# Performance work log

Measured on AMD Instinct MI355X. Metric: run time of the kernel, lower is better.

## Reference

```python
import jax, jax.numpy as jnp
import numpy as np

# ---- config constants (must match init_kwargs) ----
B, S, D, H, HD = 2, 2048, 512, 8, 64
N_BLK, L_BLK = 64, 32          # block_size, block_len (S = N_BLK*L_BLK)
R, RM = 8, 4                   # router_size, group_router_mul_factor
LN, GN, GE, GT = 8, 4, 16, 2   # moe layers, groups, group experts, topk per token
DR, DG = 128, 128
FFH = 1024
THETA = 10000.0
EPS = 1e-6

_INV_FREQ = (1.0 / THETA) ** (np.arange(0, HD, 2, dtype=np.float32) / HD)


def rmsnorm(x, w):
    return x * jax.lax.rsqrt(jnp.mean(x * x, axis=-1, keepdims=True) + EPS) * w


def rope(x):
    # x: (b, h, s, hd); y1 = x1*cos + x2*sin, y2 = -x1*sin + x2*cos (as in RotaryEmb)
    s = x.shape[2]
    freqs = jnp.outer(jnp.arange(s, dtype=jnp.float32), jnp.asarray(_INV_FREQ))[None, None]
    cos, sin = jnp.cos(freqs), jnp.sin(freqs)
    x1, x2 = jnp.split(x, 2, axis=-1)
    return jnp.concatenate([x1 * cos + x2 * sin, -x1 * sin + x2 * cos], axis=-1)


def layer(x, mask, qkv_w, o_w, up_w, down_w, n1, n2):
    b, s, d = x.shape
    xn = rmsnorm(x, n1)
    q, k, v = jnp.split(xn @ qkv_w, 3, axis=-1)
    sh = lambda t: t.reshape(b, s, H, HD).transpose(0, 2, 1, 3)  # b h s hd
    q, k, v = rope(sh(q)), rope(sh(k)), sh(v)
    scores = jnp.einsum('bhqa,bhka->bhqk', q, k) / np.sqrt(HD).astype(np.float32)
    if mask is not None:
        scores = jnp.where(mask[:, None], scores, -jnp.inf)
    p = jax.nn.softmax(scores, axis=-1)
    o = jnp.einsum('bhqk,bhka->bhqa', p, v).transpose(0, 2, 1, 3).reshape(b, s, d)
    x = x + o @ o_w
    xn2 = rmsnorm(x, n2)
    h1, h2 = jnp.split(xn2 @ up_w, 2, axis=-1)
    return x + (jax.nn.silu(h1) * h2) @ down_w


def _l2n(t, axis):
    return t / jnp.maximum(jnp.linalg.norm(t, axis=axis, keepdims=True), 1e-12)


def forward(x, doc, router_token, out_w, keys_router, keys_gate,
            enc_qkv, enc_o, enc_up, enc_down, enc_n1, enc_n2,
            rtr_qkv, rtr_o, rtr_up, rtr_down, rtr_n1, rtr_n2):
    # ---- AuxEncoder: block-causal AND same-document mask (global_attn branch) ----
    qb = jnp.arange(S) // N_BLK
    causal = qb[:, None] >= qb[None, :]                       # (S, S)
    mask = causal[None] & (doc[:, :, None] == doc[:, None, :])  # (B, S, S)
    for i in range(enc_qkv.shape[0]):
        x = layer(x, mask, enc_qkv[i], enc_o[i], enc_up[i], enc_down[i], enc_n1[i], enc_n2[i])

    # ---- AuxRouter: split into blocks, append router tokens, full attention ----
    xr = x.reshape(B * L_BLK, N_BLK, D)
    rt = jnp.broadcast_to(router_token, (B * L_BLK, R, D))
    xr = jnp.concatenate([xr, rt], axis=1)                    # (B*L, N+R, D)
    for i in range(rtr_qkv.shape[0]):
        xr = layer(xr, None, rtr_qkv[i], rtr_o[i], rtr_up[i], rtr_down[i], rtr_n1[i], rtr_n2[i])
    out = xr[:, N_BLK:] @ out_w                               # (B*L, R, DR+DG)
    xro, xgo = out[..., :DR], out[..., DR:]

    def expand(t, dd):
        # repeat '(b l) r d -> (r rm) b l d', roll(1, dim=2), flatten(1,2)
        t = t.reshape(B, L_BLK, R, dd).transpose(2, 0, 1, 3)  # (R, B, L, d)
        t = jnp.repeat(t, RM, axis=0)                          # (R*RM, B, L, d)
        t = jnp.roll(t, 1, axis=2)
        return t.reshape(R * RM, B * L_BLK, dd)

    xrr = _l2n(expand(xro, DR), -1)
    xgg = _l2n(expand(xgo, DG), -1)
    kr = _l2n(keys_router, 1)
    kg = _l2n(keys_gate, 1)
    rl = jnp.einsum('gbd,gde->gbe', xrr, kr)                  # (LN*GN, B*L, GE)
    gl = jnp.einsum('gbd,gde->gbe', xgg, kg)
    _, idx = jax.lax.top_k(rl, GT)                            # (LN*GN, B*L, GT)
    rv = jnp.take_along_axis(rl, idx, axis=-1)
    gv = jnp.take_along_axis(gl, idx, axis=-1)
    return jnp.stack([rv, gv], axis=0)                        # (2, 32, 64, 2)


def setup_inputs() -> dict:
    key = jax.random.key(0)
    ks = jax.random.split(key, 20)
    w = lambda k, shp: 0.02 * jax.random.normal(k, shp, dtype=jnp.float32)
    return {
        'x': jax.random.normal(ks[0], (B, S, D), dtype=jnp.float32),
        'doc': jnp.sort(jax.random.randint(ks[1], (B, S), 0, 4), axis=-1),
        'router_token': jax.random.normal(ks[2], (1, R, D), dtype=jnp.float32),
        'out_w': w(ks[3], (D, DR + DG)),
        'keys_router': jax.random.normal(ks[4], (LN * GN, DR, GE), dtype=jnp.float32),
        'keys_gate': jax.random.normal(ks[5], (LN * GN, DG, GE), dtype=jnp.float32),
        'enc_qkv': w(ks[6], (4, D, 3 * D)),
        'enc_o': w(ks[7], (4, D, D)),
        'enc_up': w(ks[8], (4, D, 2 * FFH)),
        'enc_down': w(ks[9], (4, FFH, D)),
        'enc_n1': jnp.ones((4, D), dtype=jnp.float32),
        'enc_n2': jnp.ones((4, D), dtype=jnp.float32),
        'rtr_qkv': w(ks[10], (2, D, 3 * D)),
        'rtr_o': w(ks[11], (2, D, D)),
        'rtr_up': w(ks[12], (2, D, 2 * FFH)),
        'rtr_down': w(ks[13], (2, FFH, D)),
        'rtr_n1': jnp.ones((2, D), dtype=jnp.float32),
        'rtr_n2': jnp.ones((2, D), dtype=jnp.float32),
    }


def reference(x, doc, router_token, out_w, keys_router, keys_gate,
              enc_qkv, enc_o, enc_up, enc_down, enc_n1, enc_n2,
              rtr_qkv, rtr_o, rtr_up, rtr_down, rtr_n1, rtr_n2):
    return forward(x, doc, router_token, out_w, keys_router, keys_gate,
                   enc_qkv, enc_o, enc_up, enc_down, enc_n1, enc_n2,
                   rtr_qkv, rtr_o, rtr_up, rtr_down, rtr_n1, rtr_n2)
```

## Files before the change

### kernel.cpp

```cpp
#include <hip/hip_runtime.h>
#include <hip/hip_bf16.h>
#include <cstdint>


typedef __attribute__((ext_vector_type(8))) short short8;
typedef __attribute__((ext_vector_type(4))) float f32x4;
typedef unsigned short ushort_t;

__device__ __forceinline__ float bf2f(unsigned short u) {
    return __uint_as_float(((unsigned)u) << 16);
}
__device__ __forceinline__ unsigned short f2bf(float f) {
    unsigned u = __float_as_uint(f);
    unsigned r = 0x7FFFu + ((u >> 16) & 1u);
    return (unsigned short)((u + r) >> 16);
}
__device__ __forceinline__ float wave_sum64(float v) {
#pragma unroll
    for (int o = 32; o; o >>= 1) v += __shfl_xor(v, o);
    return v;
}
__device__ __forceinline__ void load_lds16(const ushort_t* g, ushort_t* l) {
    __builtin_amdgcn_global_load_lds(
        (const __attribute__((address_space(1))) unsigned int*)g,
        (__attribute__((address_space(3))) unsigned int*)l, 16, 0, 0);
}

#define MFMA16(a, b, c) __builtin_amdgcn_mfma_f32_16x16x32_bf16(a, b, c, 0, 0, 0)
#define BARRIER_RAW() do { asm volatile("" ::: "memory"); \
    __builtin_amdgcn_s_barrier(); asm volatile("" ::: "memory"); } while (0)
#define VMCNT0() asm volatile("s_waitcnt vmcnt(0)" ::: "memory")

__global__ void copy_in_kernel(const float* __restrict__ src,
                               float* __restrict__ dst, int n) {
    int i = blockIdx.x * 256 + threadIdx.x;
    if (i < n) dst[i] = src[i];
}

__global__ __launch_bounds__(256) void wsplit_kernel(const float* __restrict__ W,
        unsigned short* __restrict__ WH, unsigned short* __restrict__ WL,
        int K, int N) {
    __shared__ float tile[32][33];
    int bn = blockIdx.x * 32, bk = blockIdx.y * 32;
    int tx = threadIdx.x & 31, ty = threadIdx.x >> 5;
#pragma unroll
    for (int i = 0; i < 4; ++i)
        tile[ty + 8 * i][tx] = W[(size_t)(bk + ty + 8 * i) * N + bn + tx];
    __syncthreads();
#pragma unroll
    for (int i = 0; i < 4; ++i) {
        int n = bn + ty + 8 * i, k = bk + tx;
        float x = tile[tx][ty + 8 * i];
        unsigned short h = f2bf(x);
        unsigned short lo = f2bf(x - bf2f(h));
        WH[(size_t)n * K + k] = h;
        WL[(size_t)n * K + k] = lo;
    }
}

__global__ __launch_bounds__(256) void rmsnorm_kernel(const float* __restrict__ X,
        const float* __restrict__ W, ushort_t* __restrict__ XNH,
        ushort_t* __restrict__ XNL) {
    int t = blockIdx.x, tid = threadIdx.x;
    const float* xr = X + (size_t)t * 512;
    float v0 = xr[tid], v1 = xr[tid + 256];
    float ss = wave_sum64(v0 * v0 + v1 * v1);
    __shared__ float red[4];
    if ((tid & 63) == 0) red[tid >> 6] = ss;
    __syncthreads();
    float tot = red[0] + red[1] + red[2] + red[3];
    float scale = rsqrtf(tot * (1.0f / 512.0f) + 1e-6f);
    float a0 = v0 * scale * W[tid];
    float a1 = v1 * scale * W[tid + 256];
    unsigned short h0 = f2bf(a0), h1 = f2bf(a1);
    size_t base = (size_t)t * 512;
    XNH[base + tid]       = h0;
    XNL[base + tid]       = f2bf(a0 - bf2f(h0));
    XNH[base + tid + 256] = h1;
    XNL[base + tid + 256] = f2bf(a1 - bf2f(h1));
}

template <int BM>
__global__ __launch_bounds__(256) void gemm3(
        const ushort_t* __restrict__ AH, const ushort_t* __restrict__ AL,
        const ushort_t* __restrict__ BH, const ushort_t* __restrict__ BL,
        const float* __restrict__ Res, float* __restrict__ C,
        int M, int N, int K) {
    constexpr int MI   = BM / 32;
    constexpr int ROWS = 2 * BM + 256;
    constexpr int LPW  = ROWS / 64;
    constexpr int SS   = ROWS * 32;
    __shared__ __align__(16) ushort_t S[2][ROWS][32];
    int tid = threadIdx.x;
    int n0 = blockIdx.x * 128, m0 = blockIdx.y * BM;
    int wid = tid >> 6, lane = tid & 63;
    int wm = (wid >> 1) * (BM / 2), wn = (wid & 1) * 64;
    int col = lane & 15, quad = lane >> 4;

    const ushort_t* gsrc[LPW];
    int ldof[LPW];
#pragma unroll
    for (int j = 0; j < LPW; ++j) {
        int e = wid * LPW + j;
        int srow = e * 16 + (lane >> 2);
        const ushort_t* gp; int rin;
        if (srow < BM)                { gp = AH + (size_t)m0 * K; rin = srow; }
        else if (srow < 2 * BM)       { gp = AL + (size_t)m0 * K; rin = srow - BM; }
        else if (srow < 2 * BM + 128) { gp = BH + (size_t)n0 * K; rin = srow - 2 * BM; }
        else                          { gp = BL + (size_t)n0 * K; rin = srow - 2 * BM - 128; }
        gsrc[j] = gp + (size_t)rin * K + ((lane & 3) ^ ((lane >> 3) & 3)) * 8;
        ldof[j] = e * 512;
    }
    ushort_t* sbase = &S[0][0][0];
    auto STAGE = [&](int set, int kc) {
        ushort_t* sb = sbase + set * SS;
#pragma unroll
        for (int j = 0; j < LPW; ++j)
            load_lds16(gsrc[j] + kc * 32, sb + ldof[j]);
    };

    int chrd = (quad ^ ((col >> 1) & 3)) * 8;
    f32x4 acc[MI][4] = {};
    int nk = K >> 5;
    STAGE(0, 0);
    VMCNT0();
    BARRIER_RAW();
    int cur = 0;
#pragma unroll 1
    for (int kc = 0; kc < nk; ++kc) {
        if (kc + 1 < nk) STAGE(cur ^ 1, kc + 1);
        const ushort_t* sb = sbase + cur * SS;
        short8 afh[MI], afl[MI], bfh[4], bfl[4];
#pragma unroll
        for (int i = 0; i < MI; ++i) {
            afh[i] = *(const short8*)(sb + (size_t)(wm + i * 16 + col) * 32 + chrd);
            afl[i] = *(const short8*)(sb + (size_t)(BM + wm + i * 16 + col) * 32 + chrd);
        }
#pragma unroll
        for (int i = 0; i < 4; ++i) {
            bfh[i] = *(const short8*)(sb + (size_t)(2 * BM + wn + i * 16 + col) * 32 + chrd);
            bfl[i] = *(const short8*)(sb + (size_t)(2 * BM + 128 + wn + i * 16 + col) * 32 + chrd);
        }
#pragma unroll
        for (int mi = 0; mi < MI; ++mi)
#pragma unroll
            for (int ni = 0; ni < 4; ++ni) {
                f32x4 c = acc[mi][ni];
                c = MFMA16(afh[mi], bfh[ni], c);
                c = MFMA16(afh[mi], bfl[ni], c);
                c = MFMA16(afl[mi], bfh[ni], c);
                acc[mi][ni] = c;
            }
        if (kc + 1 < nk) {
            VMCNT0();
            BARRIER_RAW();
            cur ^= 1;
        }
    }
#pragma unroll
    for (int mi = 0; mi < MI; ++mi)
#pragma unroll
        for (int ni = 0; ni < 4; ++ni)
#pragma unroll
            for (int r = 0; r < 4; ++r) {
                int row = m0 + wm + mi * 16 + quad * 4 + r;
                int ccol = n0 + wn + ni * 16 + col;
                size_t o = (size_t)row * N + ccol;
                float v = acc[mi][ni][r];
                if (Res) v += Res[o];
                C[o] = v;
            }
}

__global__ __launch_bounds__(512, 4) void gemm3w(
        const ushort_t* __restrict__ AH, const ushort_t* __restrict__ AL,
        const ushort_t* __restrict__ BH, const ushort_t* __restrict__ BL,
        const float* __restrict__ Res, float* __restrict__ C,
        int M, int N, int K) {
    constexpr int ROWS = 512;
    constexpr int LPW  = 4;
    constexpr int SS   = ROWS * 32;
    __shared__ __align__(16) ushort_t S[2][ROWS][32];
    int tid = threadIdx.x;
    int n0 = blockIdx.x * 128, m0 = blockIdx.y * 128;
    int wid = tid >> 6, lane = tid & 63;
    int wm = (wid >> 1) * 32, wn = (wid & 1) * 64;
    int col = lane & 15, quad = lane >> 4;

    const ushort_t* gsrc[LPW];
    int ldof[LPW];
#pragma unroll
    for (int j = 0; j < LPW; ++j) {
        int e = wid * LPW + j;
        int srow = e * 16 + (lane >> 2);
        const ushort_t* gp; int rin;
        if (srow < 128)      { gp = AH; rin = m0 + srow; }
        else if (srow < 256) { gp = AL; rin = m0 + srow - 128; }
        else if (srow < 384) { gp = BH; rin = n0 + srow - 256; }
        else                 { gp = BL; rin = n0 + srow - 384; }
        gsrc[j] = gp + (size_t)rin * K + ((lane & 3) ^ ((lane >> 3) & 3)) * 8;
        ldof[j] = e * 512;
    }
    ushort_t* sbase = &S[0][0][0];
    auto STAGE = [&](int set, int kc) {
        ushort_t* sb = sbase + set * SS;
#pragma unroll
        for (int j = 0; j < LPW; ++j)
            load_lds16(gsrc[j] + kc * 32, sb + ldof[j]);
    };

    int chrd = (quad ^ ((col >> 1) & 3)) * 8;
    f32x4 acc[2][4] = {};
    int nk = K >> 5;
    STAGE(0, 0);
    VMCNT0();
    BARRIER_RAW();
    int cur = 0;
#pragma unroll 1
    for (int kc = 0; kc < nk; ++kc) {
        if (kc + 1 < nk) STAGE(cur ^ 1, kc + 1);
        const ushort_t* sb = sbase + cur * SS;
        short8 afh[2], afl[2], bfh[4], bfl[4];
#pragma unroll
        for (int i = 0; i < 2; ++i) {
            afh[i] = *(const short8*)(sb + (size_t)(wm + i * 16 + col) * 32 + chrd);
            afl[i] = *(const short8*)(sb + (size_t)(128 + wm + i * 16 + col) * 32 + chrd);
        }
#pragma unroll
        for (int i = 0; i < 4; ++i) {
            bfh[i] = *(const short8*)(sb + (size_t)(256 + wn + i * 16 + col) * 32 + chrd);
            bfl[i] = *(const short8*)(sb + (size_t)(384 + wn + i * 16 + col) * 32 + chrd);
        }
#pragma unroll
        for (int mi = 0; mi < 2; ++mi)
#pragma unroll
            for (int ni = 0; ni < 4; ++ni) {
                f32x4 c = acc[mi][ni];
                c = MFMA16(afh[mi], bfh[ni], c);
                c = MFMA16(afh[mi], bfl[ni], c);
                c = MFMA16(afl[mi], bfh[ni], c);
                acc[mi][ni] = c;
            }
        if (kc + 1 < nk) {
            VMCNT0();
            BARRIER_RAW();
            cur ^= 1;
        }
    }
#pragma unroll
    for (int mi = 0; mi < 2; ++mi)
#pragma unroll
        for (int ni = 0; ni < 4; ++ni)
#pragma unroll
            for (int r = 0; r < 4; ++r) {
                int row = m0 + wm + mi * 16 + quad * 4 + r;
                int ccol = n0 + wn + ni * 16 + col;
                size_t o = (size_t)row * N + ccol;
                float v = acc[mi][ni][r];
                if (Res) v += Res[o];
                C[o] = v;
            }
}

__global__ __launch_bounds__(512, 4) void gemm_up_silu(
        const ushort_t* __restrict__ AH, const ushort_t* __restrict__ AL,
        const ushort_t* __restrict__ BH, const ushort_t* __restrict__ BL,
        ushort_t* __restrict__ MIDH, ushort_t* __restrict__ MIDL, int K) {
    constexpr int ROWS = 512;
    constexpr int LPW  = 4;
    constexpr int SS   = ROWS * 32;
    __shared__ __align__(16) ushort_t S[2][ROWS][32];
    int tid = threadIdx.x;
    int n0 = blockIdx.x * 64, m0 = blockIdx.y * 128;
    int wid = tid >> 6, lane = tid & 63;
    int wm = (wid >> 1) * 32, wn = (wid & 1) * 32;
    int col = lane & 15, quad = lane >> 4;

    const ushort_t* gsrc[LPW];
    int ldof[LPW];
#pragma unroll
    for (int j = 0; j < LPW; ++j) {
        int e = wid * LPW + j;
        int srow = e * 16 + (lane >> 2);
        const ushort_t* gp; int rin;
        if (srow < 128)      { gp = AH; rin = m0 + srow; }
        else if (srow < 256) { gp = AL; rin = m0 + srow - 128; }
        else if (srow < 320) { gp = BH; rin = n0 + srow - 256; }
        else if (srow < 384) { gp = BL; rin = n0 + srow - 320; }
        else if (srow < 448) { gp = BH; rin = 1024 + n0 + srow - 384; }
        else                 { gp = BL; rin = 1024 + n0 + srow - 448; }
        gsrc[j] = gp + (size_t)rin * K + ((lane & 3) ^ ((lane >> 3) & 3)) * 8;
        ldof[j] = e * 512;
    }
    ushort_t* sbase = &S[0][0][0];
    auto STAGE = [&](int set, int kc) {
        ushort_t* sb = sbase + set * SS;
#pragma unroll
        for (int j = 0; j < LPW; ++j)
            load_lds16(gsrc[j] + kc * 32, sb + ldof[j]);
    };

    int chrd = (quad ^ ((col >> 1) & 3)) * 8;
    f32x4 a1[2][2] = {}, a2[2][2] = {};
    int nk = K >> 5;
    STAGE(0, 0);
    VMCNT0();
    BARRIER_RAW();
    int cur = 0;
#pragma unroll 1
    for (int kc = 0; kc < nk; ++kc) {
        if (kc + 1 < nk) STAGE(cur ^ 1, kc + 1);
        const ushort_t* sb = sbase + cur * SS;
        short8 afh[2], afl[2], b1h[2], b1l[2], b2h[2], b2l[2];
#pragma unroll
        for (int i = 0; i < 2; ++i) {
            afh[i] = *(const short8*)(sb + (size_t)(wm + i * 16 + col) * 32 + chrd);
            afl[i] = *(const short8*)(sb + (size_t)(128 + wm + i * 16 + col) * 32 + chrd);
            b1h[i] = *(const short8*)(sb + (size_t)(256 + wn + i * 16 + col) * 32 + chrd);
            b1l[i] = *(const short8*)(sb + (size_t)(320 + wn + i * 16 + col) * 32 + chrd);
            b2h[i] = *(const short8*)(sb + (size_t)(384 + wn + i * 16 + col) * 32 + chrd);
            b2l[i] = *(const short8*)(sb + (size_t)(448 + wn + i * 16 + col) * 32 + chrd);
        }
#pragma unroll
        for (int mi = 0; mi < 2; ++mi)
#pragma unroll
            for (int ni = 0; ni < 2; ++ni) {
                f32x4 c = a1[mi][ni];
                c = MFMA16(afh[mi], b1h[ni], c);
                c = MFMA16(afh[mi], b1l[ni], c);
                c = MFMA16(afl[mi], b1h[ni], c);
                a1[mi][ni] = c;
                f32x4 d = a2[mi][ni];
                d = MFMA16(afh[mi], b2h[ni], d);
                d = MFMA16(afh[mi], b2l[ni], d);
                d = MFMA16(afl[mi], b2h[ni], d);
                a2[mi][ni] = d;
            }
        if (kc + 1 < nk) {
            VMCNT0();
            BARRIER_RAW();
            cur ^= 1;
        }
    }
#pragma unroll
    for (int mi = 0; mi < 2; ++mi)
#pragma unroll
        for (int ni = 0; ni < 2; ++ni)
#pragma unroll
            for (int r = 0; r < 4; ++r) {
                int row = m0 + wm + mi * 16 + quad * 4 + r;
                int ccol = n0 + wn + ni * 16 + col;
                float v1 = a1[mi][ni][r], v2 = a2[mi][ni][r];
                float rr = (v1 / (1.0f + __expf(-v1))) * v2;
                unsigned short h = f2bf(rr);
                size_t o = (size_t)row * 1024 + ccol;
                MIDH[o] = h;
                MIDL[o] = f2bf(rr - bf2f(h));
            }
}

__global__ void rope_pack_kernel(const float* __restrict__ QKV,
        float* __restrict__ Q, ushort_t* __restrict__ KH,
        ushort_t* __restrict__ KL, int Sg, int total) {
    int idx = blockIdx.x * 256 + threadIdx.x;
    if (idx >= total) return;
    int i = idx & 31;
    int h = (idx >> 5) & 7;
    int t = idx >> 8;
    int g = t / Sg; int s = t - g * Sg;
    const float* row = QKV + (size_t)t * 1536;
    float inv = powf(10000.0f, -(float)(2 * i) / 64.0f);
    float sn, cs;
    sincosf((float)s * inv, &sn, &cs);
    size_t ob = ((size_t)(g * 8 + h) * Sg + s) * 64 + i;
    int c = h * 64 + i;
    float q1 = row[c], q2 = row[c + 32];
    Q[ob]      = q1 * cs + q2 * sn;
    Q[ob + 32] = q2 * cs - q1 * sn;
    float k1 = row[512 + c], k2 = row[512 + c + 32];
    float ka = k1 * cs + k2 * sn;
    float kb = k2 * cs - k1 * sn;
    unsigned short ha = f2bf(ka), hb = f2bf(kb);
    KH[ob]      = ha;  KL[ob]      = f2bf(ka - bf2f(ha));
    KH[ob + 32] = hb;  KL[ob + 32] = f2bf(kb - bf2f(hb));
}

__global__ __launch_bounds__(256) void vtrans_kernel(const float* __restrict__ QKV,
        ushort_t* __restrict__ VTH, ushort_t* __restrict__ VTL, int Sg) {
    __shared__ float tile[64][65];
    int chunk = blockIdx.x, gh = blockIdx.y;
    int g = gh >> 3, h = gh & 7;
    int tid = threadIdx.x;
    int sr = tid >> 2, dc = (tid & 3) * 16;
    int s = chunk * 64 + sr;
    if (s < Sg) {
        const float* src = QKV + ((size_t)g * Sg + s) * 1536 + 1024 + h * 64 + dc;
#pragma unroll
        for (int j = 0; j < 4; ++j) {
            float4 v = *(const float4*)(src + 4 * j);
            tile[sr][dc + 4 * j]     = v.x;
            tile[sr][dc + 4 * j + 1] = v.y;
            tile[sr][dc + 4 * j + 2] = v.z;
            tile[sr][dc + 4 * j + 3] = v.w;
        }
    } else {
#pragma unroll
        for (int j = 0; j < 16; ++j) tile[sr][dc + j] = 0.f;
    }
    __syncthreads();
    int dr = tid >> 2, sc = (tid & 3) * 16;
    short8 hv[2], lv[2];
#pragma unroll
    for (int half = 0; half < 2; ++half)
#pragma unroll
        for (int j = 0; j < 8; ++j) {
            float v = tile[sc + half * 8 + j][dr];
            unsigned short hb = f2bf(v);
            hv[half][j] = (short)hb;
            lv[half][j] = (short)f2bf(v - bf2f(hb));
        }
    int scol = chunk * 64 + sc;
    size_t ob = ((size_t)gh * 64 + dr) * Sg + scol;
    if (scol + 16 <= Sg) {
        *(short8*)(VTH + ob)     = hv[0];
        *(short8*)(VTH + ob + 8) = hv[1];
        *(short8*)(VTL + ob)     = lv[0];
        *(short8*)(VTL + ob + 8) = lv[1];
    } else {
#pragma unroll
        for (int j = 0; j < 16; ++j)
            if (scol + j < Sg) {
                VTH[ob + j] = (ushort_t)((j < 8) ? hv[0][j] : hv[1][j - 8]);
                VTL[ob + j] = (ushort_t)((j < 8) ? lv[0][j] : lv[1][j - 8]);
            }
    }
}

template <bool MASKED>
__global__ __launch_bounds__(256, 3) void attn3_kernel(const float* __restrict__ Q,
        const ushort_t* __restrict__ KHg, const ushort_t* __restrict__ KLg,
        const ushort_t* __restrict__ VTHg, const ushort_t* __restrict__ VTLg,
        const int* __restrict__ doc, ushort_t* __restrict__ AOH,
        ushort_t* __restrict__ AOL, int Sg) {
    __shared__ __align__(16) ushort_t Khs[64][64], Kls[64][64];
    __shared__ __align__(16) ushort_t Vts[64][64], Vtl[64][64];
    __shared__ __align__(16) ushort_t Ph[4][16][72], Pl[4][16][72];
    __shared__ int dock[64];
    __shared__ int dmax_s[32];
    int qb = (int)(gridDim.x - 1 - blockIdx.x);
    int gh = blockIdx.y, g = gh >> 3;
    int tid = threadIdx.x, wid = tid >> 6, lane = tid & 63;
    int col = lane & 15, quad = lane >> 4;

    int rL = lane >> 3, cSw = (lane & 7) ^ rL;
    const ushort_t* kb;
    const ushort_t* vb;
    ushort_t* lb;
    if (wid == 0)      { kb = KHg + (size_t)gh * Sg * 64 + cSw * 8;  vb = nullptr; lb = &Khs[0][0]; }
    else if (wid == 1) { kb = KLg + (size_t)gh * Sg * 64 + cSw * 8;  vb = nullptr; lb = &Kls[0][0]; }
    else if (wid == 2) { vb = VTHg + ((size_t)gh * 64 + rL) * Sg;    kb = nullptr; lb = &Vts[0][0]; }
    else               { vb = VTLg + ((size_t)gh * 64 + rL) * Sg;    kb = nullptr; lb = &Vtl[0][0]; }
    int sw0 = ((0 + quad) ^ (col & 7)) * 8;
    int sw1 = ((4 + quad) ^ (col & 7)) * 8;

    short8 qa[2][2];
    {
        int qrow = qb * 64 + wid * 16 + col;
        if (qrow >= Sg) qrow = Sg - 1;
        const float* Qg = Q + ((size_t)gh * Sg + qrow) * 64 + quad * 8;
#pragma unroll
        for (int kk = 0; kk < 2; ++kk) {
            float4 v0 = *(const float4*)(Qg + kk * 32);
            float4 v1 = *(const float4*)(Qg + kk * 32 + 4);
            float vv[8] = {v0.x, v0.y, v0.z, v0.w, v1.x, v1.y, v1.z, v1.w};
            short8 h, l;
#pragma unroll
            for (int e = 0; e < 8; ++e) {
                float x = vv[e] * 0.125f;
                unsigned short hb = f2bf(x);
                h[e] = (short)hb;
                l[e] = (short)f2bf(x - bf2f(hb));
            }
            qa[kk][0] = h; qa[kk][1] = l;
        }
    }
    int dqr[4]; int wq0 = 0, wq1 = 0, bq0 = 0;
    int kts = 0;
    if (MASKED) {
        const int* db = doc + (size_t)g * Sg + qb * 64;
#pragma unroll
        for (int r = 0; r < 4; ++r) dqr[r] = db[wid * 16 + quad * 4 + r];
        wq0 = db[wid * 16]; wq1 = db[wid * 16 + 15];
        bq0 = db[0];
        int nkb = (Sg + 63) >> 6;
        if (tid < nkb) dmax_s[tid] = doc[(size_t)g * Sg + tid * 64 + 63];
        __syncthreads();
        int kbv = 0;
        while (kbv < nkb && dmax_s[kbv] < bq0) ++kbv;
        kts = kbv;
    }
    float m[4], l[4];
    f32x4 accO[4];
#pragma unroll
    for (int r = 0; r < 4; ++r) { m[r] = -1e30f; l[r] = 0.f; }
#pragma unroll
    for (int nd = 0; nd < 4; ++nd) accO[nd] = (f32x4){0.f, 0.f, 0.f, 0.f};

    int nkt = MASKED ? (qb + 1) : ((Sg + 63) >> 6);
    for (int kt = kts; kt < nkt; ++kt) {
        int kval = Sg - kt * 64; if (kval > 64) kval = 64;
        __syncthreads();
        if (wid < 2) {
#pragma unroll
            for (int p = 0; p < 8; ++p) {
                int sr2 = kt * 64 + p * 8 + rL;
                if (sr2 > Sg - 1) sr2 = Sg - 1;
                load_lds16(kb + (size_t)sr2 * 64, lb + p * 512);
            }
        } else {
            int vc = kt * 64 + cSw * 8;
            if (vc > Sg - 8) vc = Sg - 8;
#pragma unroll
            for (int p = 0; p < 8; ++p)
                load_lds16(vb + (size_t)(p * 8) * Sg + vc, lb + p * 512);
        }
        if (MASKED && tid < 64) dock[tid] = doc[(size_t)g * Sg + kt * 64 + tid];
        __syncthreads();
        bool wskip = false;
        if (MASKED) wskip = (dock[kval - 1] < wq0);
        if (!wskip) {
            int dk[4];
            if (MASKED) {
#pragma unroll
                for (int ni = 0; ni < 4; ++ni) dk[ni] = dock[ni * 16 + col];
            }
            f32x4 sc[4];
            __builtin_amdgcn_s_setprio(1);
#pragma unroll
            for (int ni = 0; ni < 4; ++ni) {
                int rb = (ni * 16 + col) * 64;
                short8 bh0 = *(const short8*)(&Khs[0][0] + rb + sw0);
                short8 bl0 = *(const short8*)(&Kls[0][0] + rb + sw0);
                short8 bh1 = *(const short8*)(&Khs[0][0] + rb + sw1);
                short8 bl1 = *(const short8*)(&Kls[0][0] + rb + sw1);
                f32x4 c = (f32x4){0.f, 0.f, 0.f, 0.f};
                c = MFMA16(qa[0][0], bh0, c);
                c = MFMA16(qa[0][0], bl0, c);
                c = MFMA16(qa[0][1], bh0, c);
                c = MFMA16(qa[1][0], bh1, c);
                c = MFMA16(qa[1][0], bl1, c);
                c = MFMA16(qa[1][1], bh1, c);
                sc[ni] = c;
            }
            __builtin_amdgcn_s_setprio(0);
            float mnew[4];
#pragma unroll
            for (int r = 0; r < 4; ++r) mnew[r] = -1e30f;
#pragma unroll
            for (int ni = 0; ni < 4; ++ni)
#pragma unroll
                for (int r = 0; r < 4; ++r) {
                    bool ok = MASKED ? (dk[ni] == dqr[r]) : (ni * 16 + col < kval);
                    float s = ok ? sc[ni][r] : -1e30f;
                    sc[ni][r] = s;
                    mnew[r] = fmaxf(mnew[r], s);
                }
#pragma unroll
            for (int r = 0; r < 4; ++r)
#pragma unroll
                for (int o = 1; o < 16; o <<= 1)
                    mnew[r] = fmaxf(mnew[r], __shfl_xor(mnew[r], o));
            float alpha[4], lsum[4];
#pragma unroll
            for (int r = 0; r < 4; ++r) {
                float M = fmaxf(m[r], mnew[r]);
                alpha[r] = __expf(m[r] - M);
                m[r] = M;
                lsum[r] = 0.f;
            }
#pragma unroll
            for (int ni = 0; ni < 4; ++ni)
#pragma unroll
                for (int r = 0; r < 4; ++r) {
                    bool ok = MASKED ? (dk[ni] == dqr[r]) : (ni * 16 + col < kval);
                    float p = ok ? __expf(sc[ni][r] - m[r]) : 0.f;
                    lsum[r] += p;
                    unsigned short h = f2bf(p);
                    Ph[wid][quad * 4 + r][ni * 16 + col] = h;
                    Pl[wid][quad * 4 + r][ni * 16 + col] = f2bf(p - bf2f(h));
                }
#pragma unroll
            for (int r = 0; r < 4; ++r) {
#pragma unroll
                for (int o = 1; o < 16; o <<= 1)
                    lsum[r] += __shfl_xor(lsum[r], o);
                l[r] = l[r] * alpha[r] + lsum[r];
            }
#pragma unroll
            for (int nd = 0; nd < 4; ++nd)
#pragma unroll
                for (int r = 0; r < 4; ++r) accO[nd][r] *= alpha[r];
            __builtin_amdgcn_s_setprio(1);
#pragma unroll
            for (int kk = 0; kk < 2; ++kk) {
                short8 pah = *(const short8*)&Ph[wid][col][kk * 32 + quad * 8];
                short8 pal = *(const short8*)&Pl[wid][col][kk * 32 + quad * 8];
                int sw = kk ? sw1 : sw0;
#pragma unroll
                for (int nd = 0; nd < 4; ++nd) {
                    int rb = (nd * 16 + col) * 64;
                    short8 vbh = *(const short8*)(&Vts[0][0] + rb + sw);
                    short8 vbl = *(const short8*)(&Vtl[0][0] + rb + sw);
                    f32x4 c = accO[nd];
                    c = MFMA16(pah, vbh, c);
                    c = MFMA16(pah, vbl, c);
                    c = MFMA16(pal, vbh, c);
                    accO[nd] = c;
                }
            }
            __builtin_amdgcn_s_setprio(0);
        }
    }
#pragma unroll
    for (int r = 0; r < 4; ++r) {
        int qrow = qb * 64 + wid * 16 + quad * 4 + r;
        if (qrow < Sg) {
            float inv = 1.0f / l[r];
            size_t base = ((size_t)g * Sg + qrow) * 512 + (gh & 7) * 64;
#pragma unroll
            for (int nd = 0; nd < 4; ++nd) {
                float val = accO[nd][r] * inv;
                unsigned short h = f2bf(val);
                AOH[base + nd * 16 + col] = h;
                AOL[base + nd * 16 + col] = f2bf(val - bf2f(h));
            }
        }
    }
}

__global__ void router_build_kernel(const float* __restrict__ X,
        const float* __restrict__ RT, float* __restrict__ X2, int total) {
    int idx = blockIdx.x * 256 + threadIdx.x;
    if (idx >= total) return;
    int d = idx & 511;
    int p = (idx >> 9) % 72;
    int g2 = idx / (72 * 512);
    X2[idx] = (p < 64) ? X[((size_t)g2 * 64 + p) * 512 + d]
                       : RT[(p - 64) * 512 + d];
}

__global__ void gather_rows_kernel(const float* __restrict__ X2,
        ushort_t* __restrict__ RRH, ushort_t* __restrict__ RRL, int total) {
    int idx = blockIdx.x * 256 + threadIdx.x;
    if (idx >= total) return;
    int d = idx & 511;
    int row = idx >> 9;
    int g2 = row >> 3, rr = row & 7;
    float v = X2[((size_t)(g2 * 72 + 64 + rr)) * 512 + d];
    unsigned short h = f2bf(v);
    RRH[idx] = h;
    RRL[idx] = f2bf(v - bf2f(h));
}

__global__ __launch_bounds__(64) void norm_half_kernel(const float* __restrict__ IN,
        float* __restrict__ OUT) {
    int b = blockIdx.x; int lane = threadIdx.x;
    size_t base = (size_t)(b >> 1) * 256 + (size_t)(b & 1) * 128;
    float v0 = IN[base + lane], v1 = IN[base + 64 + lane];
    float ss = wave_sum64(v0 * v0 + v1 * v1);
    float sc = 1.0f / fmaxf(sqrtf(ss), 1e-12f);
    OUT[base + lane]      = v0 * sc;
    OUT[base + 64 + lane] = v1 * sc;
}

__global__ __launch_bounds__(64) void norm_keys_kernel(const float* __restrict__ Kin,
        float* __restrict__ Kout) {
    int b = blockIdx.x; int lane = threadIdx.x;
    int g = b >> 4, e = b & 15;
    size_t base = (size_t)g * 2048 + e;
    float v0 = Kin[base + (size_t)lane * 16];
    float v1 = Kin[base + (size_t)(lane + 64) * 16];
    float ss = wave_sum64(v0 * v0 + v1 * v1);
    float sc = 1.0f / fmaxf(sqrtf(ss), 1e-12f);
    Kout[base + (size_t)lane * 16]        = v0 * sc;
    Kout[base + (size_t)(lane + 64) * 16] = v1 * sc;
}

__global__ __launch_bounds__(64) void logits_top2_kernel(const float* __restrict__ OUTN,
        const float* __restrict__ KRN, const float* __restrict__ KGN,
        float* __restrict__ out) {
    int blk = blockIdx.x;
    int g = blk >> 6, bcol = blk & 63;
    int b = bcol >> 5, l = bcol & 31;
    int lsrc = (l + 31) & 31;
    int r = g >> 2;
    int row = (b * 32 + lsrc) * 8 + r;
    const float* rvec = OUTN + (size_t)row * 256;
    __shared__ float sc[32];
    int lane = threadIdx.x;
    if (lane < 32) {
        int e = lane & 15;
        const float* kb = ((lane < 16) ? KRN : KGN) + (size_t)g * 2048 + e;
        const float* xv = (lane < 16) ? rvec : (rvec + 128);
        float s = 0.f;
#pragma unroll 8
        for (int d = 0; d < 128; ++d) s = fmaf(xv[d], kb[(size_t)d * 16], s);
        sc[lane] = s;
    }
    __syncthreads();
    if (lane == 0) {
        float bv = -1e30f, sv = -1e30f; int bi = 0, si = 0;
#pragma unroll
        for (int e = 0; e < 16; ++e) {
            float v = sc[e];
            if (v > bv) { sv = bv; si = bi; bv = v; bi = e; }
            else if (v > sv) { sv = v; si = e; }
        }
        size_t base = (size_t)g * 128 + (size_t)bcol * 2;
        out[base]            = bv;
        out[base + 1]        = sv;
        out[4096 + base]     = sc[16 + bi];
        out[4096 + base + 1] = sc[16 + si];
    }
}

static void run_layer(float* X, float* BIG, float* Qb,
                      ushort_t* KHb, ushort_t* KLb, ushort_t* VTHb, ushort_t* VTLb,
                      ushort_t* XNH, ushort_t* XNL, ushort_t* AOH, ushort_t* AOL,
                      ushort_t* MIDH, ushort_t* MIDL,
                      const unsigned short* WH, const unsigned short* WL,
                      const float* n1, const float* n2,
                      const int* doc, int G, int Sg, hipStream_t stream) {
    const size_t oQKV = 0, oO = 786432, oUP = 1048576, oDN = 2097152;
    int T = G * Sg;
    rmsnorm_kernel<<<T, 256, 0, stream>>>(X, n1, XNH, XNL);
    gemm3w<<<dim3(12, T / 128), 512, 0, stream>>>(XNH, XNL, WH + oQKV, WL + oQKV, nullptr, BIG, T, 1536, 512);
    int rp = T * 256;
    rope_pack_kernel<<<(rp + 255) / 256, 256, 0, stream>>>(BIG, Qb, KHb, KLb, Sg, rp);
    int qblocks = (Sg + 63) >> 6;
    vtrans_kernel<<<dim3(qblocks, G * 8), 256, 0, stream>>>(BIG, VTHb, VTLb, Sg);
    if (doc)
        attn3_kernel<true><<<dim3(qblocks, G * 8), 256, 0, stream>>>(Qb, KHb, KLb, VTHb, VTLb, doc, AOH, AOL, Sg);
    else
        attn3_kernel<false><<<dim3(qblocks, G * 8), 256, 0, stream>>>(Qb, KHb, KLb, VTHb, VTLb, nullptr, AOH, AOL, Sg);
    gemm3<64><<<dim3(4, T / 64), 256, 0, stream>>>(AOH, AOL, WH + oO, WL + oO, X, X, T, 512, 512);
    rmsnorm_kernel<<<T, 256, 0, stream>>>(X, n2, XNH, XNL);
    gemm_up_silu<<<dim3(16, T / 128), 512, 0, stream>>>(XNH, XNL, WH + oUP, WL + oUP, MIDH, MIDL, 512);
    gemm3<64><<<dim3(4, T / 64), 256, 0, stream>>>(MIDH, MIDL, WH + oDN, WL + oDN, X, X, T, 512, 1024);
}

static void split_layer(const float* qkv, const float* o, const float* up, const float* dn,
                        unsigned short* WH, unsigned short* WL, hipStream_t stream) {
    const size_t oQKV = 0, oO = 786432, oUP = 1048576, oDN = 2097152;
    wsplit_kernel<<<dim3(48, 16), 256, 0, stream>>>(qkv, WH + oQKV, WL + oQKV, 512, 1536);
    wsplit_kernel<<<dim3(16, 16), 256, 0, stream>>>(o,   WH + oO,   WL + oO,   512, 512);
    wsplit_kernel<<<dim3(64, 16), 256, 0, stream>>>(up,  WH + oUP,  WL + oUP,  512, 2048);
    wsplit_kernel<<<dim3(16, 32), 256, 0, stream>>>(dn,  WH + oDN,  WL + oDN,  1024, 512);
}

extern "C" void kernel_launch(void* const* d_in, const int* in_sizes, int n_in,
                              void* d_out, int out_size, void* d_ws, size_t ws_size,
                              hipStream_t stream) {
    const float* x_in    = (const float*)d_in[0];
    const int*   doc     = (const int*)d_in[1];
    const float* rt      = (const float*)d_in[2];
    const float* out_w   = (const float*)d_in[3];
    const float* k_rt    = (const float*)d_in[4];
    const float* k_gt    = (const float*)d_in[5];
    const float* enc_qkv = (const float*)d_in[6];
    const float* enc_o   = (const float*)d_in[7];
    const float* enc_up  = (const float*)d_in[8];
    const float* enc_dn  = (const float*)d_in[9];
    const float* enc_n1  = (const float*)d_in[10];
    const float* enc_n2  = (const float*)d_in[11];
    const float* rtr_qkv = (const float*)d_in[12];
    const float* rtr_o   = (const float*)d_in[13];
    const float* rtr_up  = (const float*)d_in[14];
    const float* rtr_dn  = (const float*)d_in[15];
    const float* rtr_n1  = (const float*)d_in[16];
    const float* rtr_n2  = (const float*)d_in[17];

    float* ws = (float*)d_ws;
    size_t off = 0;
    auto alloc = [&](size_t n) { float* p = ws + off; off += n; return p; };
    float* X    = alloc(4608UL * 512);
    float* X2   = alloc(4608UL * 512);
    float* BIG  = alloc(4608UL * 2048);
    float* Qb   = alloc(4608UL * 512);
    ushort_t* KHb  = (ushort_t*)alloc(1179648UL);
    ushort_t* KLb  = (ushort_t*)alloc(1179648UL);
    ushort_t* VTHb = (ushort_t*)alloc(1179648UL);
    ushort_t* VTLb = (ushort_t*)alloc(1179648UL);
    unsigned short* WH = (unsigned short*)(ws + off);
    unsigned short* WL = WH + 2621440UL;
    off += 2621440UL;
    ushort_t* XNH = (ushort_t*)Qb;
    ushort_t* XNL = XNH + 4608UL * 512;
    ushort_t* AOH = (ushort_t*)BIG;
    ushort_t* AOL = AOH + 4608UL * 512;
    ushort_t* MIDH = (ushort_t*)BIG;
    ushort_t* MIDL = MIDH + 4608UL * 1024;
    ushort_t* RRH = (ushort_t*)X;
    ushort_t* RRL = RRH + 262144;
    float* OUTM = X + 262144;
    float* OUTN = X + 393216;
    float* KRN  = X + 524288;
    float* KGN  = X + 589824;
    (void)ws_size; (void)in_sizes; (void)n_in; (void)out_size;

    copy_in_kernel<<<(2097152 + 255) / 256, 256, 0, stream>>>(x_in, X, 2097152);

    for (int i = 0; i < 4; ++i) {
        split_layer(enc_qkv + (size_t)i * 512 * 1536,
                    enc_o   + (size_t)i * 512 * 512,
                    enc_up  + (size_t)i * 512 * 2048,
                    enc_dn  + (size_t)i * 1024 * 512, WH, WL, stream);
        run_layer(X, BIG, Qb, KHb, KLb, VTHb, VTLb, XNH, XNL, AOH, AOL, MIDH, MIDL,
                  WH, WL, enc_n1 + (size_t)i * 512, enc_n2 + (size_t)i * 512,
                  doc, 2, 2048, stream);
    }

    int rb_total = 64 * 72 * 512;
    router_build_kernel<<<(rb_total + 255) / 256, 256, 0, stream>>>(X, rt, X2, rb_total);

    for (int i = 0; i < 2; ++i) {
        split_layer(rtr_qkv + (size_t)i * 512 * 1536,
                    rtr_o   + (size_t)i * 512 * 512,
                    rtr_up  + (size_t)i * 512 * 2048,
                    rtr_dn  + (size_t)i * 1024 * 512, WH, WL, stream);
        run_layer(X2, BIG, Qb, KHb, KLb, VTHb, VTLb, XNH, XNL, AOH, AOL, MIDH, MIDL,
                  WH, WL, rtr_n1 + (size_t)i * 512, rtr_n2 + (size_t)i * 512,
                  nullptr, 64, 72, stream);
    }

    gather_rows_kernel<<<(512 * 512) / 256, 256, 0, stream>>>(X2, RRH, RRL, 512 * 512);
    wsplit_kernel<<<dim3(8, 16), 256, 0, stream>>>(out_w, WH, WL, 512, 256);
    gemm3<64><<<dim3(2, 8), 256, 0, stream>>>(RRH, RRL, WH, WL, nullptr, OUTM, 512, 256, 512);

    norm_half_kernel<<<1024, 64, 0, stream>>>(OUTM, OUTN);
    norm_keys_kernel<<<512, 64, 0, stream>>>(k_rt, KRN);
    norm_keys_kernel<<<512, 64, 0, stream>>>(k_gt, KGN);
    logits_top2_kernel<<<2048, 64, 0, stream>>>(OUTN, KRN, KGN, (float*)d_out);
}
```

Baseline: 1.230 ms.

## Triple-buffer GEMM loads, shrink up-silu tiles, one-wave-per-row rmsnorm

The gemm3 and gemm_up_silu kernels move from double to triple-buffered LDS staging with two chunks in flight, waiting on a partial vmcnt instead of draining all loads, so global latency overlaps compute. gemm_up_silu drops to 256 threads with 64-row tiles, doubling the grid. rmsnorm now handles one row per wave with no shared-memory reduction or block barrier, four rows per block. The cost is more LDS per block, which may reduce occupancy, and vmcnt values that depend on the exact per-thread load count.

```diff
diff --git a/kernel.cpp b/kernel.cpp
--- a/kernel.cpp
+++ b/kernel.cpp
@@ -61,23 +61,23 @@
 __global__ __launch_bounds__(256) void rmsnorm_kernel(const float* __restrict__ X,
         const float* __restrict__ W, ushort_t* __restrict__ XNH,
         ushort_t* __restrict__ XNL) {
-    int t = blockIdx.x, tid = threadIdx.x;
+    int w = threadIdx.x >> 6, lane = threadIdx.x & 63;
+    int t = blockIdx.x * 4 + w;
     const float* xr = X + (size_t)t * 512;
-    float v0 = xr[tid], v1 = xr[tid + 256];
-    float ss = wave_sum64(v0 * v0 + v1 * v1);
-    __shared__ float red[4];
-    if ((tid & 63) == 0) red[tid >> 6] = ss;
-    __syncthreads();
-    float tot = red[0] + red[1] + red[2] + red[3];
-    float scale = rsqrtf(tot * (1.0f / 512.0f) + 1e-6f);
-    float a0 = v0 * scale * W[tid];
-    float a1 = v1 * scale * W[tid + 256];
-    unsigned short h0 = f2bf(a0), h1 = f2bf(a1);
+    float v[8];
+    float ss = 0.f;
+#pragma unroll
+    for (int j = 0; j < 8; ++j) { v[j] = xr[lane + 64 * j]; ss += v[j] * v[j]; }
+    ss = wave_sum64(ss);
+    float scale = rsqrtf(ss * (1.0f / 512.0f) + 1e-6f);
     size_t base = (size_t)t * 512;
-    XNH[base + tid]       = h0;
-    XNL[base + tid]       = f2bf(a0 - bf2f(h0));
-    XNH[base + tid + 256] = h1;
-    XNL[base + tid + 256] = f2bf(a1 - bf2f(h1));
+#pragma unroll
+    for (int j = 0; j < 8; ++j) {
+        float a = v[j] * scale * W[lane + 64 * j];
+        unsigned short h = f2bf(a);
+        XNH[base + lane + 64 * j] = h;
+        XNL[base + lane + 64 * j] = f2bf(a - bf2f(h));
+    }
 }
 
 template <int BM>
@@ -90,7 +90,7 @@
     constexpr int ROWS = 2 * BM + 256;
     constexpr int LPW  = ROWS / 64;
     constexpr int SS   = ROWS * 32;
-    __shared__ __align__(16) ushort_t S[2][ROWS][32];
+    __shared__ __align__(16) ushort_t S[3][ROWS][32];
     int tid = threadIdx.x;
     int n0 = blockIdx.x * 128, m0 = blockIdx.y * BM;
     int wid = tid >> 6, lane = tid & 63;
@@ -118,18 +118,23 @@
         for (int j = 0; j < LPW; ++j)
             load_lds16(gsrc[j] + kc * 32, sb + ldof[j]);
     };
+    auto WAITK = [&]() {
+        if constexpr (BM == 64) asm volatile("s_waitcnt vmcnt(6)" ::: "memory");
+        else                    asm volatile("s_waitcnt vmcnt(8)" ::: "memory");
+    };
 
     int chrd = (quad ^ ((col >> 1) & 3)) * 8;
     f32x4 acc[MI][4] = {};
     int nk = K >> 5;
     STAGE(0, 0);
-    VMCNT0();
+    if (nk > 1) { STAGE(1, 1); WAITK(); }
+    else        { VMCNT0(); }
     BARRIER_RAW();
-    int cur = 0;
+    int sc = 0, sn = 1, sp = 2;
 #pragma unroll 1
     for (int kc = 0; kc < nk; ++kc) {
-        if (kc + 1 < nk) STAGE(cur ^ 1, kc + 1);
-        const ushort_t* sb = sbase + cur * SS;
+        if (kc + 2 < nk) STAGE(sp, kc + 2);
+        const ushort_t* sb = sbase + sc * SS;
         short8 afh[MI], afl[MI], bfh[4], bfl[4];
 #pragma unroll
         for (int i = 0; i < MI; ++i) {
@@ -152,10 +157,11 @@
                 acc[mi][ni] = c;
             }
         if (kc + 1 < nk) {
-            VMCNT0();
+            if (kc + 2 < nk) WAITK();
+            else VMCNT0();
             BARRIER_RAW();
-            cur ^= 1;
-        }
+        }
+        int t = sc; sc = sn; sn = sp; sp = t;
     }
 #pragma unroll
     for (int mi = 0; mi < MI; ++mi)
@@ -262,16 +268,16 @@
             }
 }
 
-__global__ __launch_bounds__(512, 4) void gemm_up_silu(
+__global__ __launch_bounds__(256) void gemm_up_silu(
         const ushort_t* __restrict__ AH, const ushort_t* __restrict__ AL,
         const ushort_t* __restrict__ BH, const ushort_t* __restrict__ BL,
         ushort_t* __restrict__ MIDH, ushort_t* __restrict__ MIDL, int K) {
-    constexpr int ROWS = 512;
-    constexpr int LPW  = 4;
+    constexpr int ROWS = 384;
+    constexpr int LPW  = 6;
     constexpr int SS   = ROWS * 32;
-    __shared__ __align__(16) ushort_t S[2][ROWS][32];
+    __shared__ __align__(16) ushort_t S[3][ROWS][32];
     int tid = threadIdx.x;
-    int n0 = blockIdx.x * 64, m0 = blockIdx.y * 128;
+    int n0 = blockIdx.x * 64, m0 = blockIdx.y * 64;
     int wid = tid >> 6, lane = tid & 63;
     int wm = (wid >> 1) * 32, wn = (wid & 1) * 32;
     int col = lane & 15, quad = lane >> 4;
@@ -283,12 +289,12 @@
         int e = wid * LPW + j;
         int srow = e * 16 + (lane >> 2);
         const ushort_t* gp; int rin;
-        if (srow < 128)      { gp = AH; rin = m0 + srow; }
-        else if (srow < 256) { gp = AL; rin = m0 + srow - 128; }
-        else if (srow < 320) { gp = BH; rin = n0 + srow - 256; }
-        else if (srow < 384) { gp = BL; rin = n0 + srow - 320; }
-        else if (srow < 448) { gp = BH; rin = 1024 + n0 + srow - 384; }
-        else                 { gp = BL; rin = 1024 + n0 + srow - 448; }
+        if (srow < 64)       { gp = AH; rin = m0 + srow; }
+        else if (srow < 128) { gp = AL; rin = m0 + srow - 64; }
+        else if (srow < 192) { gp = BH; rin = n0 + srow - 128; }
+        else if (srow < 256) { gp = BL; rin = n0 + srow - 192; }
+        else if (srow < 320) { gp = BH; rin = 1024 + n0 + srow - 256; }
+        else                 { gp = BL; rin = 1024 + n0 + srow - 320; }
         gsrc[j] = gp + (size_t)rin * K + ((lane & 3) ^ ((lane >> 3) & 3)) * 8;
         ldof[j] = e * 512;
     }
@@ -299,27 +305,29 @@
         for (int j = 0; j < LPW; ++j)
             load_lds16(gsrc[j] + kc * 32, sb + ldof[j]);
     };
+    auto WAITK = [&]() { asm volatile("s_waitcnt vmcnt(6)" ::: "memory"); };
 
     int chrd = (quad ^ ((col >> 1) & 3)) * 8;
     f32x4 a1[2][2] = {}, a2[2][2] = {};
     int nk = K >> 5;
     STAGE(0, 0);
-    VMCNT0();
+    if (nk > 1) { STAGE(1, 1); WAITK(); }
+    else        { VMCNT0(); }
     BARRIER_RAW();
-    int cur = 0;
+    int sc = 0, sn = 1, sp = 2;
 #pragma unroll 1
     for (int kc = 0; kc < nk; ++kc) {
-        if (kc + 1 < nk) STAGE(cur ^ 1, kc + 1);
-        const ushort_t* sb = sbase + cur * SS;
+        if (kc + 2 < nk) STAGE(sp, kc + 2);
+        const ushort_t* sb = sbase + sc * SS;
         short8 afh[2], afl[2], b1h[2], b1l[2], b2h[2], b2l[2];
 #pragma unroll
         for (int i = 0; i < 2; ++i) {
             afh[i] = *(const short8*)(sb + (size_t)(wm + i * 16 + col) * 32 + chrd);
-            afl[i] = *(const short8*)(sb + (size_t)(128 + wm + i * 16 + col) * 32 + chrd);
-            b1h[i] = *(const short8*)(sb + (size_t)(256 + wn + i * 16 + col) * 32 + chrd);
-            b1l[i] = *(const short8*)(sb + (size_t)(320 + wn + i * 16 + col) * 32 + chrd);
-            b2h[i] = *(const short8*)(sb + (size_t)(384 + wn + i * 16 + col) * 32 + chrd);
-            b2l[i] = *(const short8*)(sb + (size_t)(448 + wn + i * 16 + col) * 32 + chrd);
+            afl[i] = *(const short8*)(sb + (size_t)(64 + wm + i * 16 + col) * 32 + chrd);
+            b1h[i] = *(const short8*)(sb + (size_t)(128 + wn + i * 16 + col) * 32 + chrd);
+            b1l[i] = *(const short8*)(sb + (size_t)(192 + wn + i * 16 + col) * 32 + chrd);
+            b2h[i] = *(const short8*)(sb + (size_t)(256 + wn + i * 16 + col) * 32 + chrd);
+            b2l[i] = *(const short8*)(sb + (size_t)(320 + wn + i * 16 + col) * 32 + chrd);
         }
 #pragma unroll
         for (int mi = 0; mi < 2; ++mi)
@@ -337,10 +345,11 @@
                 a2[mi][ni] = d;
             }
         if (kc + 1 < nk) {
-            VMCNT0();
+            if (kc + 2 < nk) WAITK();
+            else VMCNT0();
             BARRIER_RAW();
-            cur ^= 1;
-        }
+        }
+        int t = sc; sc = sn; sn = sp; sp = t;
     }
 #pragma unroll
     for (int mi = 0; mi < 2; ++mi)
@@ -733,7 +742,7 @@
                       const int* doc, int G, int Sg, hipStream_t stream) {
     const size_t oQKV = 0, oO = 786432, oUP = 1048576, oDN = 2097152;
     int T = G * Sg;
-    rmsnorm_kernel<<<T, 256, 0, stream>>>(X, n1, XNH, XNL);
+    rmsnorm_kernel<<<T / 4, 256, 0, stream>>>(X, n1, XNH, XNL);
     gemm3w<<<dim3(12, T / 128), 512, 0, stream>>>(XNH, XNL, WH + oQKV, WL + oQKV, nullptr, BIG, T, 1536, 512);
     int rp = T * 256;
     rope_pack_kernel<<<(rp + 255) / 256, 256, 0, stream>>>(BIG, Qb, KHb, KLb, Sg, rp);
@@ -744,8 +753,8 @@
     else
         attn3_kernel<false><<<dim3(qblocks, G * 8), 256, 0, stream>>>(Qb, KHb, KLb, VTHb, VTLb, nullptr, AOH, AOL, Sg);
     gemm3<64><<<dim3(4, T / 64), 256, 0, stream>>>(AOH, AOL, WH + oO, WL + oO, X, X, T, 512, 512);
-    rmsnorm_kernel<<<T, 256, 0, stream>>>(X, n2, XNH, XNL);
-    gemm_up_silu<<<dim3(16, T / 128), 512, 0, stream>>>(XNH, XNL, WH + oUP, WL + oUP, MIDH, MIDL, 512);
+    rmsnorm_kernel<<<T / 4, 256, 0, stream>>>(X, n2, XNH, XNL);
+    gemm_up_silu<<<dim3(16, T / 64), 256, 0, stream>>>(XNH, XNL, WH + oUP, WL + oUP, MIDH, MIDL, 512);
     gemm3<64><<<dim3(4, T / 64), 256, 0, stream>>>(MIDH, MIDL, WH + oDN, WL + oDN, X, X, T, 512, 1024);
 }
 
```

New measurement: 1.215 ms. Within noise of the previous version (-1.2%).
